# Kernel optimization log

Measured on AMD Instinct MI355X. Metric: run time of the kernel, lower is better.

## Reference

```python
import jax, jax.numpy as jnp
import numpy as np

# --- 3D Sobel kernels (smoothing [1,2,1] x derivative [-1,0,1]) ---
_H = np.array([1.0, 2.0, 1.0], np.float32)
_G = np.array([-1.0, 0.0, 1.0], np.float32)
SOBEL_X = jnp.asarray(np.einsum('i,j,k->ijk', _H, _H, _G))  # deriv along W
SOBEL_Y = jnp.asarray(np.einsum('i,j,k->ijk', _H, _G, _H))  # deriv along H
SOBEL_Z = jnp.asarray(np.einsum('i,j,k->ijk', _G, _H, _H))  # deriv along D

UPDATE_RATE = 0.25
ALIVE_THRESH = 0.1


def _depthwise3d(xp, kern3, C):
    # xp: [B,C,D+2,H+2,W+2] circular-padded; kern3: [3,3,3] shared across channels
    k = jnp.broadcast_to(kern3[None, None], (C, 1, 3, 3, 3))
    return jax.lax.conv_general_dilated(
        xp, k, window_strides=(1, 1, 1), padding='VALID',
        dimension_numbers=('NCDHW', 'OIDHW', 'NCDHW'), feature_group_count=C)


def setup_inputs() -> dict:
    key = jax.random.key(0)
    k1, k2, k3, k4, k5 = jax.random.split(key, 5)
    B, C, S = 8, 16, 64
    HID = 32
    x = jax.random.normal(k1, (B, C, S, S, S), dtype=jnp.float32)
    rand_mask = jax.random.uniform(k2, (B, C, S, S, S), dtype=jnp.float32)
    # 1x1 conv weights, init normal(std=0.001) as in the torch module
    W1 = 0.001 * jax.random.normal(k3, (HID, 4 * C), dtype=jnp.float32)
    b1 = 0.001 * jax.random.normal(k4, (HID,), dtype=jnp.float32)
    W2 = 0.001 * jax.random.normal(k5, (C, HID), dtype=jnp.float32)
    return {"x": x, "rand_mask": rand_mask, "W1": W1, "b1": b1, "W2": W2}


def reference(x, rand_mask, W1, b1, W2):
    B, C, D, H, W = x.shape
    # perception: circular pad + depthwise sobel convs, concat with identity
    xp = jnp.pad(x, ((0, 0), (0, 0), (1, 1), (1, 1), (1, 1)), mode='wrap')
    gx = _depthwise3d(xp, SOBEL_X, C)
    gy = _depthwise3d(xp, SOBEL_Y, C)
    gz = _depthwise3d(xp, SOBEL_Z, C)
    perc = jnp.concatenate([gx, gy, gz, x], axis=1)  # [B,4C,D,H,W]
    # 1x1 conv MLP
    h = jax.nn.relu(jnp.einsum('bcdhw,oc->bodhw', perc, W1)
                    + b1[None, :, None, None, None])
    dy = jnp.einsum('bcdhw,oc->bodhw', h, W2)  # [B,C,D,H,W]
    # stochastic update mask: floor(rand + rate) is 1 with prob rate
    upd = jnp.floor(rand_mask + UPDATE_RATE)
    y = x + dy * upd
    # alive mask: 3x3x3 max pool (zero... -inf pad) on alpha channel 3
    alpha = y[:, 3]  # [B,D,H,W]
    pooled = jax.lax.reduce_window(
        alpha, -jnp.inf, jax.lax.max, (1, 3, 3, 3), (1, 1, 1, 1),
        [(0, 0), (1, 1), (1, 1), (1, 1)])
    alive = (pooled > ALIVE_THRESH).astype(y.dtype)
    return y * alive[:, None]
```

## Files before the change

kernel.cpp:

```cpp
#include <hip/hip_runtime.h>
#include <math.h>

#define SD   64
#define NC   16
#define NHID 32
#define NB   8
#define ALIVE_T 0.1f

__global__ __launch_bounds__(256, 4) void nca_step(
    const float* __restrict__ x, const float* __restrict__ rm,
    const float* __restrict__ W1, const float* __restrict__ b1,
    const float* __restrict__ W2, float* __restrict__ y,
    float* __restrict__ alpha)
{
    const int lane = threadIdx.x & 63;
    const int r    = blockIdx.x * 4 + (threadIdx.x >> 6);
    const int h    = r & 63;
    const int d    = (r >> 6) & 63;
    const int b    = r >> 12;

    const int dm = (d + 63) & 63, dp = (d + 1) & 63;
    const int hm = (h + 63) & 63, hp = (h + 1) & 63;
    const int lm = (lane + 63) & 63, lp = (lane + 1) & 63;

    const int o_mm = (dm << 12) + (hm << 6) + lane;
    const int o_m0 = (dm << 12) + (h  << 6) + lane;
    const int o_mp = (dm << 12) + (hp << 6) + lane;
    const int o_0m = (d  << 12) + (hm << 6) + lane;
    const int o_00 = (d  << 12) + (h  << 6) + lane;
    const int o_0p = (d  << 12) + (hp << 6) + lane;
    const int o_pm = (dp << 12) + (hm << 6) + lane;
    const int o_p0 = (dp << 12) + (h  << 6) + lane;
    const int o_pp = (dp << 12) + (hp << 6) + lane;

    float hacc[NHID];
    #pragma unroll
    for (int o = 0; o < NHID; ++o) hacc[o] = b1[o];

    float xv[NC];

    #pragma unroll
    for (int c = 0; c < NC; ++c) {
        const float* base = x + (((size_t)(b * NC + c)) << 18);
        float v_mm = base[o_mm], v_m0 = base[o_m0], v_mp = base[o_mp];
        float v_0m = base[o_0m], v_00 = base[o_00], v_0p = base[o_0p];
        float v_pm = base[o_pm], v_p0 = base[o_p0], v_pp = base[o_pp];
        float am = v_mm + 2.f * v_m0 + v_mp;
        float a0 = v_0m + 2.f * v_00 + v_0p;
        float ap = v_pm + 2.f * v_p0 + v_pp;
        float gm = v_mp - v_mm;
        float g0 = v_0p - v_0m;
        float gp = v_pp - v_pm;
        float P_hh = am + 2.f * a0 + ap;
        float P_hg = gm + 2.f * g0 + gp;
        float P_gh = ap - am;
        float gx = __shfl(P_hh, lp, 64) - __shfl(P_hh, lm, 64);
        float gy = __shfl(P_hg, lm, 64) + 2.f * P_hg + __shfl(P_hg, lp, 64);
        float gz = __shfl(P_gh, lm, 64) + 2.f * P_gh + __shfl(P_gh, lp, 64);
        xv[c] = v_00;
        #pragma unroll
        for (int o = 0; o < NHID; ++o) {
            float t = fmaf(W1[(o << 6) + c],          gx,   hacc[o]);
            t       = fmaf(W1[(o << 6) + NC + c],     gy,   t);
            t       = fmaf(W1[(o << 6) + 2 * NC + c], gz,   t);
            hacc[o] = fmaf(W1[(o << 6) + 3 * NC + c], v_00, t);
        }
    }

    float dyv[NC];
    #pragma unroll
    for (int ch = 0; ch < NC; ++ch) dyv[ch] = 0.f;
    #pragma unroll
    for (int o = 0; o < NHID; ++o) {
        float a = fmaxf(hacc[o], 0.f);
        #pragma unroll
        for (int ch = 0; ch < NC; ++ch)
            dyv[ch] = fmaf(W2[(ch << 5) + o], a, dyv[ch]);
    }

    const size_t voff = ((size_t)d << 12) + ((size_t)h << 6) + lane;
    #pragma unroll
    for (int ch = 0; ch < NC; ++ch) {
        const size_t idx = (((size_t)(b * NC + ch)) << 18) + voff;
        float upd = floorf(rm[idx] + 0.25f);
        float yv  = fmaf(dyv[ch], upd, xv[ch]);
        y[idx] = yv;
        if (ch == 3) alpha[(((size_t)b) << 18) + voff] = yv;
    }
}

__global__ __launch_bounds__(256, 4) void alive_mask(
    const float* __restrict__ alpha, float* __restrict__ y)
{
    const int tid  = blockIdx.x * 256 + threadIdx.x;
    const int lane = threadIdx.x & 63;
    const int wq   = tid & 15;
    const int w4   = wq << 2;
    const int h    = (tid >> 4) & 63;
    const int d    = (tid >> 10) & 63;
    const int b    = tid >> 16;

    const float* ab = alpha + (((size_t)b) << 18);

    float m0 = -INFINITY, m1 = -INFINITY, m2 = -INFINITY, m3 = -INFINITY;
    #pragma unroll
    for (int dz = -1; dz <= 1; ++dz) {
        int dd = d + dz;
        if (dd < 0 || dd > 63) continue;
        #pragma unroll
        for (int hy = -1; hy <= 1; ++hy) {
            int hh = h + hy;
            if (hh < 0 || hh > 63) continue;
            const float4 v = *reinterpret_cast<const float4*>(
                ab + (dd << 12) + (hh << 6) + w4);
            m0 = fmaxf(m0, v.x); m1 = fmaxf(m1, v.y);
            m2 = fmaxf(m2, v.z); m3 = fmaxf(m3, v.w);
        }
    }
    float left  = __shfl(m3, (lane + 63) & 63, 64);
    float right = __shfl(m0, (lane + 1) & 63, 64);
    if (wq == 0)  left  = -INFINITY;
    if (wq == 15) right = -INFINITY;

    float p0 = fmaxf(left, fmaxf(m0, m1));
    float p1 = fmaxf(m0,   fmaxf(m1, m2));
    float p2 = fmaxf(m1,   fmaxf(m2, m3));
    float p3 = fmaxf(m2,   fmaxf(m3, right));

    const bool d0 = !(p0 > ALIVE_T);
    const bool d1 = !(p1 > ALIVE_T);
    const bool d2 = !(p2 > ALIVE_T);
    const bool d3 = !(p3 > ALIVE_T);

    if (d0 | d1 | d2 | d3) {
        const size_t voff = ((size_t)d << 12) + ((size_t)h << 6) + w4;
        #pragma unroll
        for (int ch = 0; ch < NC; ++ch) {
            float* p = y + (((size_t)(b * NC + ch)) << 18) + voff;
            if (d0) p[0] = 0.f;
            if (d1) p[1] = 0.f;
            if (d2) p[2] = 0.f;
            if (d3) p[3] = 0.f;
        }
    }
}

extern "C" void kernel_launch(void* const* d_in, const int* in_sizes, int n_in,
                              void* d_out, int out_size, void* d_ws, size_t ws_size,
                              hipStream_t stream) {
    const float* x  = (const float*)d_in[0];
    const float* rm = (const float*)d_in[1];
    const float* W1 = (const float*)d_in[2];
    const float* b1 = (const float*)d_in[3];
    const float* W2 = (const float*)d_in[4];
    float* y     = (float*)d_out;
    float* alpha = (float*)d_ws;

    const int rows    = NB * SD * SD;
    const int blocks1 = rows / 4;
    const int blocks2 = (NB * SD * SD * 16) / 256;

    nca_step<<<blocks1, 256, 0, stream>>>(x, rm, W1, b1, W2, y, alpha);
    alive_mask<<<blocks2, 256, 0, stream>>>(alpha, y);
}
```

Before: 401.0 us.

## Run both 1x1-conv MLP layers on bf16 MFMA via per-wave LDS staging

Replaces the scalar FMA loops for the two pointwise layers with bf16 MFMA 16x16x32 instructions. Each wave packs its perception features into a wave-private LDS tile as bf16, runs the 64->32 and 32->16 matmuls as MFMAs, and reads dy back from LDS. This targets the large per-thread FMA count and the register pressure of the per-voxel MLP. In exchange it lowers precision to bf16 for weights, features and hidden activations, and adds LDS traffic without barriers, which relies on each wave owning its tile.

```diff
diff --git a/kernel.cpp b/kernel.cpp
--- a/kernel.cpp
+++ b/kernel.cpp
@@ -1,4 +1,5 @@
 #include <hip/hip_runtime.h>
+#include <hip/hip_bf16.h>
 #include <math.h>
 
 #define SD   64
@@ -6,6 +7,18 @@
 #define NHID 32
 #define NB   8
 #define ALIVE_T 0.1f
+#define LSTR 160
+
+typedef float        f32x4  __attribute__((ext_vector_type(4)));
+typedef short        bf16x8 __attribute__((ext_vector_type(8)));
+typedef unsigned int u32x2  __attribute__((ext_vector_type(2)));
+
+static __device__ __forceinline__ unsigned short f2bf(float f) {
+    return __builtin_bit_cast(unsigned short, __float2bfloat16(f));
+}
+static __device__ __forceinline__ unsigned pack2(float lo, float hi) {
+    return (unsigned)f2bf(lo) | ((unsigned)f2bf(hi) << 16);
+}
 
 __global__ __launch_bounds__(256, 4) void nca_step(
     const float* __restrict__ x, const float* __restrict__ rm,
@@ -13,11 +26,48 @@
     const float* __restrict__ W2, float* __restrict__ y,
     float* __restrict__ alpha)
 {
-    const int lane = threadIdx.x & 63;
-    const int r    = blockIdx.x * 4 + (threadIdx.x >> 6);
+    const int tid  = threadIdx.x;
+    const int lane = tid & 63;
+    const int wid  = tid >> 6;
+    const int r    = blockIdx.x * 4 + wid;
     const int h    = r & 63;
     const int d    = (r >> 6) & 63;
     const int b    = r >> 12;
+
+    const int lg = lane >> 4;
+    const int ln = lane & 15;
+
+    __shared__ __align__(16) unsigned char lds_all[4][64 * LSTR];
+    unsigned char* lds   = lds_all[wid];
+    unsigned char* myrow = lds + lane * LSTR;
+
+    bf16x8 a1[2][2];
+    #pragma unroll
+    for (int mt = 0; mt < 2; ++mt)
+      #pragma unroll
+      for (int ks = 0; ks < 2; ++ks) {
+        const float* wp = W1 + (ln + 16 * mt) * 64 + ks * 32 + lg * 8;
+        f32x4 w0 = *(const f32x4*)wp;
+        f32x4 w1 = *(const f32x4*)(wp + 4);
+        bf16x8 f;
+        f[0]=(short)f2bf(w0[0]); f[1]=(short)f2bf(w0[1]);
+        f[2]=(short)f2bf(w0[2]); f[3]=(short)f2bf(w0[3]);
+        f[4]=(short)f2bf(w1[0]); f[5]=(short)f2bf(w1[1]);
+        f[6]=(short)f2bf(w1[2]); f[7]=(short)f2bf(w1[3]);
+        a1[mt][ks] = f;
+      }
+    bf16x8 a2;
+    {
+        const float* wp = W2 + ln * 32 + lg * 8;
+        f32x4 w0 = *(const f32x4*)wp;
+        f32x4 w1 = *(const f32x4*)(wp + 4);
+        a2[0]=(short)f2bf(w0[0]); a2[1]=(short)f2bf(w0[1]);
+        a2[2]=(short)f2bf(w0[2]); a2[3]=(short)f2bf(w0[3]);
+        a2[4]=(short)f2bf(w1[0]); a2[5]=(short)f2bf(w1[1]);
+        a2[6]=(short)f2bf(w1[2]); a2[7]=(short)f2bf(w1[3]);
+    }
+    const f32x4 b1lo = *(const f32x4*)(b1 + lg * 4);
+    const f32x4 b1hi = *(const f32x4*)(b1 + 16 + lg * 4);
 
     const int dm = (d + 63) & 63, dp = (d + 1) & 63;
     const int hm = (h + 63) & 63, hp = (h + 1) & 63;
@@ -33,49 +83,88 @@
     const int o_p0 = (dp << 12) + (h  << 6) + lane;
     const int o_pp = (dp << 12) + (hp << 6) + lane;
 
-    float hacc[NHID];
-    #pragma unroll
-    for (int o = 0; o < NHID; ++o) hacc[o] = b1[o];
-
     float xv[NC];
 
     #pragma unroll
-    for (int c = 0; c < NC; ++c) {
-        const float* base = x + (((size_t)(b * NC + c)) << 18);
-        float v_mm = base[o_mm], v_m0 = base[o_m0], v_mp = base[o_mp];
-        float v_0m = base[o_0m], v_00 = base[o_00], v_0p = base[o_0p];
-        float v_pm = base[o_pm], v_p0 = base[o_p0], v_pp = base[o_pp];
-        float am = v_mm + 2.f * v_m0 + v_mp;
-        float a0 = v_0m + 2.f * v_00 + v_0p;
-        float ap = v_pm + 2.f * v_p0 + v_pp;
-        float gm = v_mp - v_mm;
-        float g0 = v_0p - v_0m;
-        float gp = v_pp - v_pm;
-        float P_hh = am + 2.f * a0 + ap;
-        float P_hg = gm + 2.f * g0 + gp;
-        float P_gh = ap - am;
-        float gx = __shfl(P_hh, lp, 64) - __shfl(P_hh, lm, 64);
-        float gy = __shfl(P_hg, lm, 64) + 2.f * P_hg + __shfl(P_hg, lp, 64);
-        float gz = __shfl(P_gh, lm, 64) + 2.f * P_gh + __shfl(P_gh, lp, 64);
-        xv[c] = v_00;
-        #pragma unroll
-        for (int o = 0; o < NHID; ++o) {
-            float t = fmaf(W1[(o << 6) + c],          gx,   hacc[o]);
-            t       = fmaf(W1[(o << 6) + NC + c],     gy,   t);
-            t       = fmaf(W1[(o << 6) + 2 * NC + c], gz,   t);
-            hacc[o] = fmaf(W1[(o << 6) + 3 * NC + c], v_00, t);
+    for (int c0 = 0; c0 < NC; c0 += 2) {
+        float fa[4], fb[4];
+        #pragma unroll
+        for (int cc = 0; cc < 2; ++cc) {
+            const int c = c0 + cc;
+            const float* base = x + (((size_t)(b * NC + c)) << 18);
+            float v_mm = base[o_mm], v_m0 = base[o_m0], v_mp = base[o_mp];
+            float v_0m = base[o_0m], v_00 = base[o_00], v_0p = base[o_0p];
+            float v_pm = base[o_pm], v_p0 = base[o_p0], v_pp = base[o_pp];
+            float am = v_mm + 2.f * v_m0 + v_mp;
+            float a0 = v_0m + 2.f * v_00 + v_0p;
+            float ap = v_pm + 2.f * v_p0 + v_pp;
+            float gm = v_mp - v_mm;
+            float g0 = v_0p - v_0m;
+            float gp = v_pp - v_pm;
+            float P_hh = am + 2.f * a0 + ap;
+            float P_hg = gm + 2.f * g0 + gp;
+            float P_gh = ap - am;
+            float gx = __shfl(P_hh, lp, 64) - __shfl(P_hh, lm, 64);
+            float gy = __shfl(P_hg, lm, 64) + 2.f * P_hg + __shfl(P_hg, lp, 64);
+            float gz = __shfl(P_gh, lm, 64) + 2.f * P_gh + __shfl(P_gh, lp, 64);
+            float* o = cc ? fb : fa;
+            o[0] = gx; o[1] = gy; o[2] = gz; o[3] = v_00;
+            xv[c] = v_00;
         }
-    }
+        *(unsigned*)(myrow +       2 * c0) = pack2(fa[0], fb[0]);
+        *(unsigned*)(myrow + 32 +  2 * c0) = pack2(fa[1], fb[1]);
+        *(unsigned*)(myrow + 64 +  2 * c0) = pack2(fa[2], fb[2]);
+        *(unsigned*)(myrow + 96 +  2 * c0) = pack2(fa[3], fb[3]);
+    }
+
+    f32x4 acc1[2][4];
+    #pragma unroll
+    for (int nt = 0; nt < 4; ++nt) { acc1[0][nt] = b1lo; acc1[1][nt] = b1hi; }
+
+    #pragma unroll
+    for (int ks = 0; ks < 2; ++ks) {
+        bf16x8 bp[4];
+        #pragma unroll
+        for (int nt = 0; nt < 4; ++nt)
+            bp[nt] = *(const bf16x8*)(lds + (ln + 16 * nt) * LSTR + ks * 64 + lg * 16);
+        #pragma unroll
+        for (int mt = 0; mt < 2; ++mt)
+          #pragma unroll
+          for (int nt = 0; nt < 4; ++nt)
+            acc1[mt][nt] = __builtin_amdgcn_mfma_f32_16x16x32_bf16(
+                a1[mt][ks], bp[nt], acc1[mt][nt], 0, 0, 0);
+    }
+
+    #pragma unroll
+    for (int mt = 0; mt < 2; ++mt)
+      #pragma unroll
+      for (int nt = 0; nt < 4; ++nt) {
+        f32x4 v = acc1[mt][nt];
+        u32x2 u;
+        u[0] = pack2(fmaxf(v[0], 0.f), fmaxf(v[1], 0.f));
+        u[1] = pack2(fmaxf(v[2], 0.f), fmaxf(v[3], 0.f));
+        *(u32x2*)(lds + (ln + 16 * nt) * LSTR + (lg * 8 + 32 * mt)) = u;
+      }
+
+    f32x4 acc2[4];
+    #pragma unroll
+    for (int nt = 0; nt < 4; ++nt) acc2[nt] = (f32x4){0.f, 0.f, 0.f, 0.f};
+    #pragma unroll
+    for (int nt = 0; nt < 4; ++nt) {
+        bf16x8 bh = *(const bf16x8*)(lds + (ln + 16 * nt) * LSTR + lg * 16);
+        acc2[nt] = __builtin_amdgcn_mfma_f32_16x16x32_bf16(a2, bh, acc2[nt], 0, 0, 0);
+    }
+
+    #pragma unroll
+    for (int nt = 0; nt < 4; ++nt)
+        *(f32x4*)(lds + (ln + 16 * nt) * LSTR + 64 + lg * 16) = acc2[nt];
 
     float dyv[NC];
     #pragma unroll
-    for (int ch = 0; ch < NC; ++ch) dyv[ch] = 0.f;
-    #pragma unroll
-    for (int o = 0; o < NHID; ++o) {
-        float a = fmaxf(hacc[o], 0.f);
-        #pragma unroll
-        for (int ch = 0; ch < NC; ++ch)
-            dyv[ch] = fmaf(W2[(ch << 5) + o], a, dyv[ch]);
+    for (int j = 0; j < 4; ++j) {
+        f32x4 t = *(const f32x4*)(myrow + 64 + j * 16);
+        dyv[4 * j + 0] = t[0]; dyv[4 * j + 1] = t[1];
+        dyv[4 * j + 2] = t[2]; dyv[4 * j + 3] = t[3];
     }
 
     const size_t voff = ((size_t)d << 12) + ((size_t)h << 6) + lane;
```

New measurement: 370.2 us. 1.08x faster.
